# Kernel tuning notes

Measured on AMD Instinct MI355X. Metric: run time of the kernel, lower is better.

## Reference

```python
import jax, jax.numpy as jnp
import numpy as np

NORM_EPS = 1e-6
QUANT_EPS = 1e-8


def setup_inputs() -> dict:
    key = jax.random.key(0)
    k1, k2 = jax.random.split(key)
    B, S, D_IN, D_OUT = 2, 4096, 2048, 2048
    x = jax.random.normal(k1, (B, S, D_IN), dtype=jnp.float32)
    # master fp32 weights (kaiming-uniform-ish scale)
    weight = jax.random.uniform(k2, (D_OUT, D_IN), dtype=jnp.float32,
                                minval=-1.0, maxval=1.0) * (1.0 / np.sqrt(D_IN))
    norm_weight = jnp.ones((D_IN,), dtype=jnp.float32)
    return {"x": x, "weight": weight, "norm_weight": norm_weight}


def _rmsnorm(x, gain):
    rms = jnp.sqrt(jnp.mean(x * x, axis=-1, keepdims=True) + NORM_EPS)
    return x / rms * gain


def _ternary_quantize(w):
    gamma = jnp.mean(jnp.abs(w))                       # absmean scale (scalar)
    w_q = jnp.clip(jnp.round(w / (gamma + QUANT_EPS)), -1.0, 1.0)
    return w_q, gamma


def reference(x, weight, norm_weight):
    # 1) RMSNorm input
    xn = _rmsnorm(x, norm_weight)
    # 2) ternary-quantize weights {-1,0,+1} with absmean gamma
    w_q, gamma = _ternary_quantize(weight)
    # 3) matmul with ternary weights, 4) scale by gamma
    # xn: [B,S,Din], w_q: [Dout,Din] -> [B,S,Dout]
    return jnp.einsum('bsd,od->bso', xn, w_q) * gamma
```

## Files before the change

### kernel.cpp

```cpp
#include <hip/hip_runtime.h>
#include <hip/hip_bf16.h>
#include <stdint.h>

typedef unsigned short u16;
typedef signed char i8;

#define D_INNER 2048
#define D_OUTER 2048
#define MROWS   8192
#define W_ELEMS (D_OUTER * D_INNER)
#define NPART   1024

#define BM 128
#define BN 128
#define BK 128

typedef __attribute__((ext_vector_type(4))) float f32x4;
typedef __attribute__((ext_vector_type(4))) int   i32x4;

__global__ __launch_bounds__(256) void prep_kernel(const float* __restrict__ x,
                            const float* __restrict__ g,
                            const float* __restrict__ w,
                            i8* __restrict__ xn, float* __restrict__ srow,
                            float* __restrict__ partials) {
  __shared__ float red[4];
  __shared__ float redm[4];
  int t = threadIdx.x;
  int lane = t & 63, wvi = t >> 6;

  if (blockIdx.x >= MROWS) {
    int p = blockIdx.x - MROWS;
    int base = p * 1024;
    float s = 0.f;
#pragma unroll
    for (int r = 0; r < 4; ++r) {
      f32x4 v = ((const f32x4*)w)[base + r * 256 + t];
      s += fabsf(v[0]) + fabsf(v[1]) + fabsf(v[2]) + fabsf(v[3]);
    }
    for (int off = 32; off; off >>= 1) s += __shfl_down(s, off, 64);
    if (lane == 0) red[wvi] = s;
    __syncthreads();
    if (t == 0) partials[p] = red[0] + red[1] + red[2] + red[3];
    return;
  }

  int row = blockIdx.x;
  const f32x4* xr = (const f32x4*)(x + (size_t)row * D_INNER);
  i8* xo = xn + (size_t)row * D_INNER;

  f32x4 v0 = __builtin_nontemporal_load(&xr[t]);
  f32x4 v1 = __builtin_nontemporal_load(&xr[t + 256]);
  const f32x4* gr = (const f32x4*)g;
  f32x4 g0 = gr[t], g1 = gr[t + 256];

  float s = v0[0]*v0[0] + v0[1]*v0[1] + v0[2]*v0[2] + v0[3]*v0[3]
          + v1[0]*v1[0] + v1[1]*v1[1] + v1[2]*v1[2] + v1[3]*v1[3];
  float m = fmaxf(fmaxf(fmaxf(fabsf(v0[0]*g0[0]), fabsf(v0[1]*g0[1])),
                        fmaxf(fabsf(v0[2]*g0[2]), fabsf(v0[3]*g0[3]))),
                  fmaxf(fmaxf(fabsf(v1[0]*g1[0]), fabsf(v1[1]*g1[1])),
                        fmaxf(fabsf(v1[2]*g1[2]), fabsf(v1[3]*g1[3]))));
  for (int off = 32; off; off >>= 1) {
    s += __shfl_down(s, off, 64);
    m = fmaxf(m, __shfl_down(m, off, 64));
  }
  if (lane == 0) { red[wvi] = s; redm[wvi] = m; }
  __syncthreads();
  float total = red[0] + red[1] + red[2] + red[3];
  float rmax  = fmaxf(fmaxf(redm[0], redm[1]), fmaxf(redm[2], redm[3]));
  float invr = 1.0f / sqrtf(total * (1.0f / (float)D_INNER) + 1e-6f);

  float amax = fmaxf(rmax * invr, 1e-12f);
  float step = amax * (1.0f / 127.0f);
  float qs   = 127.0f / amax;
  if (t == 0) srow[row] = step;

  char4 q0, q1;
  float qv;
  qv = fminf(127.f, fmaxf(-127.f, rintf(v0[0]*invr*g0[0]*qs))); q0.x = (i8)(int)qv;
  qv = fminf(127.f, fmaxf(-127.f, rintf(v0[1]*invr*g0[1]*qs))); q0.y = (i8)(int)qv;
  qv = fminf(127.f, fmaxf(-127.f, rintf(v0[2]*invr*g0[2]*qs))); q0.z = (i8)(int)qv;
  qv = fminf(127.f, fmaxf(-127.f, rintf(v0[3]*invr*g0[3]*qs))); q0.w = (i8)(int)qv;
  qv = fminf(127.f, fmaxf(-127.f, rintf(v1[0]*invr*g1[0]*qs))); q1.x = (i8)(int)qv;
  qv = fminf(127.f, fmaxf(-127.f, rintf(v1[1]*invr*g1[1]*qs))); q1.y = (i8)(int)qv;
  qv = fminf(127.f, fmaxf(-127.f, rintf(v1[2]*invr*g1[2]*qs))); q1.z = (i8)(int)qv;
  qv = fminf(127.f, fmaxf(-127.f, rintf(v1[3]*invr*g1[3]*qs))); q1.w = (i8)(int)qv;
  ((char4*)xo)[t]       = q0;
  ((char4*)xo)[t + 256] = q1;
}

__global__ __launch_bounds__(256) void quant_kernel(const float* __restrict__ w,
                             const float* __restrict__ partials,
                             float* __restrict__ gamma_out, i8* __restrict__ wq) {
  f32x4 pv = ((const f32x4*)partials)[threadIdx.x];
  double d = (double)pv[0] + (double)pv[1] + (double)pv[2] + (double)pv[3];
  for (int off = 32; off; off >>= 1) d += __shfl_down(d, off, 64);
  __shared__ double red[4];
  int lane = threadIdx.x & 63, wvi = threadIdx.x >> 6;
  if (lane == 0) red[wvi] = d;
  __syncthreads();
  double total = red[0] + red[1] + red[2] + red[3];
  float gamma = (float)(total * (1.0 / (double)W_ELEMS));
  float inv = 1.0f / (gamma + 1e-8f);
  if (blockIdx.x == 0 && threadIdx.x == 0) *gamma_out = gamma;

  int tid = blockIdx.x * blockDim.x + threadIdx.x;
  int stride = gridDim.x * blockDim.x;
  for (int i = tid; i < W_ELEMS / 4; i += stride) {
    f32x4 v = ((const f32x4*)w)[i];
    char4 q;
    q.x = (i8)(int)fminf(1.f, fmaxf(-1.f, rintf(v[0] * inv)));
    q.y = (i8)(int)fminf(1.f, fmaxf(-1.f, rintf(v[1] * inv)));
    q.z = (i8)(int)fminf(1.f, fmaxf(-1.f, rintf(v[2] * inv)));
    q.w = (i8)(int)fminf(1.f, fmaxf(-1.f, rintf(v[3] * inv)));
    ((char4*)wq)[i] = q;
  }
}

__global__ __launch_bounds__(256) void gemm_bt(const i8* __restrict__ A,
                                               const i8* __restrict__ Bw,
                                               const float* __restrict__ gamma_p,
                                               const float* __restrict__ srow,
                                               float* __restrict__ C) {
  __shared__ __align__(16) i8 As[BM * BK];
  __shared__ __align__(16) i8 Bs[BN * BK];

  int f   = blockIdx.y * 16 + blockIdx.x;
  int xcd = f & 7;
  int gg  = f >> 3;
  int nb  = (xcd >> 2) * 8 + (gg & 7);
  int mb  = (gg >> 3) * 4 + (xcd & 3);
  int bm0 = mb * BM;
  int bn0 = nb * BN;

  int tid  = threadIdx.x;
  int lane = tid & 63;
  int wv   = tid >> 6;
  int wm   = (wv >> 1) * 64;
  int wn   = (wv & 1) * 64;
  int lm   = lane & 15;
  int kg   = lane >> 4;
  int sw   = lm & 7;

  i32x4 acc[4][4] = {};

  const i8* Ag = A  + (size_t)bm0 * D_INNER;
  const i8* Bg = Bw + (size_t)bn0 * D_INNER;

  for (int kt = 0; kt < D_INNER; kt += BK) {
    __syncthreads();
#pragma unroll
    for (int r = 0; r < 4; ++r) {
      int ci = r * 256 + tid;
      int row = ci >> 3;
      int kc = (((ci & 7) ^ (row & 7)) << 4);
      __builtin_amdgcn_global_load_lds(
          (const __attribute__((address_space(1))) void*)(Ag + (size_t)row * D_INNER + kt + kc),
          (__attribute__((address_space(3))) void*)(As + ci * 16), 16, 0, 0);
    }
#pragma unroll
    for (int r = 0; r < 4; ++r) {
      int ci = r * 256 + tid;
      int row = ci >> 3;
      int kc = (((ci & 7) ^ (row & 7)) << 4);
      __builtin_amdgcn_global_load_lds(
          (const __attribute__((address_space(1))) void*)(Bg + (size_t)row * D_INNER + kt + kc),
          (__attribute__((address_space(3))) void*)(Bs + ci * 16), 16, 0, 0);
    }
    __syncthreads();

#pragma unroll
    for (int s = 0; s < 2; ++s) {
      int gsel = s * 4 + kg;
      i32x4 af[4], bb[4];
#pragma unroll
      for (int i = 0; i < 4; ++i)
        af[i] = *(const i32x4*)(As + (wm + i * 16 + lm) * BK + ((gsel ^ sw) << 4));
#pragma unroll
      for (int j = 0; j < 4; ++j)
        bb[j] = *(const i32x4*)(Bs + (wn + j * 16 + lm) * BK + ((gsel ^ sw) << 4));
#pragma unroll
      for (int i = 0; i < 4; ++i)
#pragma unroll
        for (int j = 0; j < 4; ++j)
          acc[i][j] = __builtin_amdgcn_mfma_i32_16x16x64_i8(af[i], bb[j], acc[i][j], 0, 0, 0);
    }
  }

  float gamma = *gamma_p;
#pragma unroll
  for (int i = 0; i < 4; ++i) {
    int row0 = bm0 + wm + i * 16 + kg * 4;
    f32x4 sv = *(const f32x4*)(srow + row0);
#pragma unroll
    for (int j = 0; j < 4; ++j) {
      int col = bn0 + wn + j * 16 + lm;
      i32x4 v = acc[i][j];
#pragma unroll
      for (int r = 0; r < 4; ++r)
        C[(size_t)(row0 + r) * D_OUTER + col] = (float)v[r] * gamma * sv[r];
    }
  }
}

extern "C" void kernel_launch(void* const* d_in, const int* in_sizes, int n_in,
                              void* d_out, int out_size, void* d_ws, size_t ws_size,
                              hipStream_t stream) {
  const float* x = (const float*)d_in[0];
  const float* w = (const float*)d_in[1];
  const float* g = (const float*)d_in[2];
  float* out = (float*)d_out;

  float* gamma_p  = (float*)d_ws;
  float* partials = (float*)((char*)d_ws + 64);
  float* srow     = (float*)((char*)d_ws + 8192);
  i8* xn = (i8*)((char*)d_ws + 8192 + 32768);
  i8* wq = (i8*)((char*)d_ws + 8192 + 32768 + (size_t)MROWS * D_INNER);

  prep_kernel<<<MROWS + NPART, 256, 0, stream>>>(x, g, w, xn, srow, partials);
  quant_kernel<<<2048, 256, 0, stream>>>(w, partials, gamma_p, wq);
  gemm_bt<<<dim3(D_OUTER / BN, MROWS / BM), 256, 0, stream>>>(xn, wq, gamma_p, srow, out);
}
```

Baseline: 169.1 us.

## Rewrite int8 GEMM with 256x256 tiles and a 4-stage async LDS pipeline

Replaces the 128x128x128 single-buffered GEMM with a 256x256x64 tile computed by 512 threads. Tiles are staged into four LDS slots with global_load_lds, using vmcnt waits to keep three tiles in flight ahead of compute. The inner product moves to 32x32x32 i8 MFMA, with s_setprio around the MFMA block. The goal is to hide global load latency and raise MFMA density. In exchange it needs 128KB of dynamic LDS, allowing one block per CU, and launches only 256 blocks.

```diff
diff --git a/kernel.cpp b/kernel.cpp
--- a/kernel.cpp
+++ b/kernel.cpp
@@ -11,12 +11,16 @@
 #define W_ELEMS (D_OUTER * D_INNER)
 #define NPART   1024
 
-#define BM 128
-#define BN 128
-#define BK 128
+#define BM 256
+#define BN 256
+#define BK 64
+#define NKT (D_INNER / BK)
+#define SLOT_BYTES 32768
+#define LDS_TOTAL  131072
 
 typedef __attribute__((ext_vector_type(4))) float f32x4;
 typedef __attribute__((ext_vector_type(4))) int   i32x4;
+typedef __attribute__((ext_vector_type(16))) int  i32x16;
 
 __global__ __launch_bounds__(256) void prep_kernel(const float* __restrict__ x,
                             const float* __restrict__ g,
@@ -116,88 +120,110 @@
   }
 }
 
-__global__ __launch_bounds__(256) void gemm_bt(const i8* __restrict__ A,
-                                               const i8* __restrict__ Bw,
-                                               const float* __restrict__ gamma_p,
-                                               const float* __restrict__ srow,
-                                               float* __restrict__ C) {
-  __shared__ __align__(16) i8 As[BM * BK];
-  __shared__ __align__(16) i8 Bs[BN * BK];
-
-  int f   = blockIdx.y * 16 + blockIdx.x;
+#define GLDS(SRC, DST) __builtin_amdgcn_global_load_lds( \
+    (const __attribute__((address_space(1))) void*)(SRC), \
+    (__attribute__((address_space(3))) void*)(DST), 16, 0, 0)
+#define WAITVM(N) asm volatile("s_waitcnt vmcnt(" #N ")" ::: "memory")
+#define BAR() asm volatile("s_barrier" ::: "memory")
+
+__global__ __launch_bounds__(512, 2) void gemm_bt(const i8* __restrict__ A,
+                                                  const i8* __restrict__ Bw,
+                                                  const float* __restrict__ gamma_p,
+                                                  const float* __restrict__ srow,
+                                                  float* __restrict__ C) {
+  extern __shared__ i8 lds[];
+
+  int f   = blockIdx.y * 8 + blockIdx.x;
   int xcd = f & 7;
-  int gg  = f >> 3;
-  int nb  = (xcd >> 2) * 8 + (gg & 7);
-  int mb  = (gg >> 3) * 4 + (xcd & 3);
+  int g   = f >> 3;
+  int orig = xcd * 32 + g;
+  int nb  = orig & 7;
+  int mb  = orig >> 3;
   int bm0 = mb * BM;
   int bn0 = nb * BN;
 
   int tid  = threadIdx.x;
   int lane = tid & 63;
   int wv   = tid >> 6;
-  int wm   = (wv >> 1) * 64;
-  int wn   = (wv & 1) * 64;
-  int lm   = lane & 15;
-  int kg   = lane >> 4;
-  int sw   = lm & 7;
-
-  i32x4 acc[4][4] = {};
+  int wr   = wv >> 2;
+  int wc   = wv & 3;
+  int l31  = lane & 31;
+  int hi   = lane >> 5;
+  int wr4  = wr * 4;
+  int wc2  = wc * 2;
 
   const i8* Ag = A  + (size_t)bm0 * D_INNER;
   const i8* Bg = Bw + (size_t)bn0 * D_INNER;
 
-  for (int kt = 0; kt < D_INNER; kt += BK) {
-    __syncthreads();
-#pragma unroll
-    for (int r = 0; r < 4; ++r) {
-      int ci = r * 256 + tid;
-      int row = ci >> 3;
-      int kc = (((ci & 7) ^ (row & 7)) << 4);
-      __builtin_amdgcn_global_load_lds(
-          (const __attribute__((address_space(1))) void*)(Ag + (size_t)row * D_INNER + kt + kc),
-          (__attribute__((address_space(3))) void*)(As + ci * 16), 16, 0, 0);
+  int srow_ = ((tid >> 6) & 7) * 32 + (tid & 31);
+  int sg_   = (tid >> 5) & 1;
+  size_t off0 = (size_t)srow_ * D_INNER + sg_ * 16;
+  int dst0 = tid * 16;
+
+  int rdoff = (hi * 32 + l31) * 16;
+
+  i32x16 acc[4][2] = {};
+
+#define STAGE(T_, S_) do { \
+    const i8* ap_ = Ag + (size_t)(T_) * BK + off0; \
+    const i8* bp_ = Bg + (size_t)(T_) * BK + off0; \
+    i8* sa_ = lds + (S_) * SLOT_BYTES + dst0; \
+    GLDS(ap_,      sa_);          \
+    GLDS(ap_ + 32, sa_ + 8192);   \
+    GLDS(bp_,      sa_ + 16384);  \
+    GLDS(bp_ + 32, sa_ + 24576);  \
+  } while (0)
+
+#define TILE_COMPUTE(T_) do { \
+    const i8* sl_ = lds + ((T_) & 3) * SLOT_BYTES; \
+    i32x4 af[2][4], bf[2][2]; \
+    _Pragma("unroll") for (int ks = 0; ks < 2; ++ks) { \
+      _Pragma("unroll") for (int mi = 0; mi < 4; ++mi) \
+        af[ks][mi] = *(const i32x4*)(sl_ + ks * 8192 + (wr4 + mi) * 1024 + rdoff); \
+      _Pragma("unroll") for (int nj = 0; nj < 2; ++nj) \
+        bf[ks][nj] = *(const i32x4*)(sl_ + 16384 + ks * 8192 + (wc2 + nj) * 1024 + rdoff); \
+    } \
+    __builtin_amdgcn_s_setprio(1); \
+    _Pragma("unroll") for (int ks = 0; ks < 2; ++ks) \
+      _Pragma("unroll") for (int mi = 0; mi < 4; ++mi) \
+        _Pragma("unroll") for (int nj = 0; nj < 2; ++nj) \
+          acc[mi][nj] = __builtin_amdgcn_mfma_i32_32x32x32_i8(af[ks][mi], bf[ks][nj], acc[mi][nj], 0, 0, 0); \
+    __builtin_amdgcn_s_setprio(0); \
+  } while (0)
+
+  STAGE(0, 0); STAGE(1, 1); STAGE(2, 2);
+
+  for (int t = 0; t < NKT - 3; ++t) {
+    STAGE(t + 3, (t + 3) & 3);
+    WAITVM(12);
+    BAR();
+    TILE_COMPUTE(t);
+    BAR();
+  }
+  WAITVM(8);  BAR(); TILE_COMPUTE(NKT - 3); BAR();
+  WAITVM(4);  BAR(); TILE_COMPUTE(NKT - 2); BAR();
+  WAITVM(0);  BAR(); TILE_COMPUTE(NKT - 1);
+
+  float gamma = *gamma_p;
+  int colb = bn0 + wc * 64 + l31;
+#pragma unroll
+  for (int mi = 0; mi < 4; ++mi) {
+    int rbase = bm0 + wr * 128 + mi * 32 + hi * 4;
+    f32x4 sg[4];
+#pragma unroll
+    for (int q = 0; q < 4; ++q) {
+      f32x4 sv = *(const f32x4*)(srow + rbase + q * 8);
+      sg[q] = sv * gamma;
     }
 #pragma unroll
-    for (int r = 0; r < 4; ++r) {
-      int ci = r * 256 + tid;
-      int row = ci >> 3;
-      int kc = (((ci & 7) ^ (row & 7)) << 4);
-      __builtin_amdgcn_global_load_lds(
-          (const __attribute__((address_space(1))) void*)(Bg + (size_t)row * D_INNER + kt + kc),
-          (__attribute__((address_space(3))) void*)(Bs + ci * 16), 16, 0, 0);
-    }
-    __syncthreads();
-
-#pragma unroll
-    for (int s = 0; s < 2; ++s) {
-      int gsel = s * 4 + kg;
-      i32x4 af[4], bb[4];
-#pragma unroll
-      for (int i = 0; i < 4; ++i)
-        af[i] = *(const i32x4*)(As + (wm + i * 16 + lm) * BK + ((gsel ^ sw) << 4));
-#pragma unroll
-      for (int j = 0; j < 4; ++j)
-        bb[j] = *(const i32x4*)(Bs + (wn + j * 16 + lm) * BK + ((gsel ^ sw) << 4));
-#pragma unroll
-      for (int i = 0; i < 4; ++i)
-#pragma unroll
-        for (int j = 0; j < 4; ++j)
-          acc[i][j] = __builtin_amdgcn_mfma_i32_16x16x64_i8(af[i], bb[j], acc[i][j], 0, 0, 0);
-    }
-  }
-
-  float gamma = *gamma_p;
-#pragma unroll
-  for (int i = 0; i < 4; ++i) {
-    int row0 = bm0 + wm + i * 16 + kg * 4;
-    f32x4 sv = *(const f32x4*)(srow + row0);
-#pragma unroll
-    for (int j = 0; j < 4; ++j) {
-      int col = bn0 + wn + j * 16 + lm;
-      i32x4 v = acc[i][j];
-#pragma unroll
-      for (int r = 0; r < 4; ++r)
-        C[(size_t)(row0 + r) * D_OUTER + col] = (float)v[r] * gamma * sv[r];
+    for (int nj = 0; nj < 2; ++nj) {
+      i32x16 v = acc[mi][nj];
+      float* cp = C + (size_t)rbase * D_OUTER + (colb + nj * 32);
+#pragma unroll
+      for (int q = 0; q < 4; ++q)
+#pragma unroll
+        for (int rr = 0; rr < 4; ++rr)
+          cp[(size_t)(q * 8 + rr) * D_OUTER] = (float)v[q * 4 + rr] * sg[q][rr];
     }
   }
 }
@@ -216,7 +242,14 @@
   i8* xn = (i8*)((char*)d_ws + 8192 + 32768);
   i8* wq = (i8*)((char*)d_ws + 8192 + 32768 + (size_t)MROWS * D_INNER);
 
+  static bool attr_set = false;
+  if (!attr_set) {
+    (void)hipFuncSetAttribute(reinterpret_cast<const void*>(&gemm_bt),
+                              hipFuncAttributeMaxDynamicSharedMemorySize, LDS_TOTAL);
+    attr_set = true;
+  }
+
   prep_kernel<<<MROWS + NPART, 256, 0, stream>>>(x, g, w, xn, srow, partials);
   quant_kernel<<<2048, 256, 0, stream>>>(w, partials, gamma_p, wq);
-  gemm_bt<<<dim3(D_OUTER / BN, MROWS / BM), 256, 0, stream>>>(xn, wq, gamma_p, srow, out);
-}
+  gemm_bt<<<dim3(8, 32), 512, LDS_TOTAL, stream>>>(xn, wq, gamma_p, srow, out);
+}
```

New measurement: 171.7 us. No clear change (+1.5%).
